# Optimization experiments

Hardware: AMD Instinct MI355X
Metric: run time of the kernel (lower is better)

Reference implementation:

```python
import jax, jax.numpy as jnp
import numpy as np

N = 50000   # num nodes
E = 800000  # num edges (avg degree 16)
D = 128     # in = hidden = out channels


def setup_inputs() -> dict:
    key = jax.random.key(0)
    k0, k1, k2, k3, k4, k5 = jax.random.split(key, 6)
    x = jax.random.normal(k0, (N, D), dtype=jnp.float32)
    edge_index = jax.random.randint(k1, (2, E), 0, N, dtype=jnp.int32)
    scale = 1.0 / np.sqrt(D)
    W1 = jax.random.normal(k2, (D, D), dtype=jnp.float32) * scale
    b1 = jax.random.normal(k3, (D,), dtype=jnp.float32) * 0.01
    W2 = jax.random.normal(k4, (D, D), dtype=jnp.float32) * scale
    b2 = jax.random.normal(k5, (D,), dtype=jnp.float32) * 0.01
    return {"x": x, "edge_index": edge_index, "W1": W1, "b1": b1, "W2": W2, "b2": b2}


def reference(x, edge_index, W1, b1, W2, b2):
    n = x.shape[0]
    src, dst = edge_index[0], edge_index[1]
    # GCN adds self-loops before normalization
    loops = jnp.arange(n, dtype=src.dtype)
    s = jnp.concatenate([src, loops])
    d = jnp.concatenate([dst, loops])
    # symmetric normalization: deg^{-1/2}[s] * deg^{-1/2}[d]
    deg = jax.ops.segment_sum(jnp.ones_like(d, dtype=x.dtype), d, num_segments=n)
    dinv = jnp.where(deg > 0, jax.lax.rsqrt(deg), 0.0)
    ew = dinv[s] * dinv[d]  # [E+N]

    def gcn_conv(h, W, b):
        h = h @ W                                   # [N, D] dense transform first
        msg = ew[:, None] * h[s]                     # gather over edges [E+N, D]
        agg = jax.ops.segment_sum(msg, d, num_segments=n)  # scatter-add [N, D]
        return agg + b

    # layer 1: conv -> Identity BN -> ELU (dropout=0.0 -> no-op)
    h = jax.nn.elu(gcn_conv(x, W1, b1))
    # layer 2 (last): conv -> Identity BN -> ELU
    out = jax.nn.elu(gcn_conv(h, W2, b2))
    return out
```

## Files before the change

### kernel.cpp

```cpp
#include <hip/hip_runtime.h>
#include <math.h>

#define D 128
#define BCAP 8192
#define SLICE 64
#define PB 256

typedef __attribute__((ext_vector_type(8))) short bf16x8;
typedef __attribute__((ext_vector_type(4))) float f32x4;


__device__ inline float2 bf2f2(unsigned int u) {
    union { unsigned int i; float f; } a, b;
    a.i = u << 16;
    b.i = u & 0xffff0000u;
    return make_float2(a.f, b.f);
}

__device__ inline unsigned short f2bf(float f) {
    union { float f; unsigned int i; } u;
    u.f = f;
    unsigned int r = u.i + 0x7fffu + ((u.i >> 16) & 1u);
    return (unsigned short)(r >> 16);
}


__device__ __forceinline__ void gemm_core(unsigned short (*Ws)[136], int gbid,
                                          const void* __restrict__ Ain, int a_fp32,
                                          unsigned int* __restrict__ Cb, int N) {
    const int tid = threadIdx.x;
    const int wid = tid >> 6;
    const int lane = tid & 63;
    const int quad = lane >> 4;
    const int ln = lane & 15;
    const int m = gbid * 64 + wid * 16 + ln;
    const bool valid = (m < N);

    f32x4 acc[8];
#pragma unroll
    for (int c = 0; c < 8; ++c) acc[c] = (f32x4){0.f, 0.f, 0.f, 0.f};

    __syncthreads();

#pragma unroll
    for (int ks = 0; ks < 4; ++ks) {
        const int k0 = ks * 32;
        bf16x8 af;
        if (a_fp32) {
            const float* A = (const float*)Ain;
            float4 lo = make_float4(0.f, 0.f, 0.f, 0.f), hi = lo;
            if (valid) {
                lo = *(const float4*)&A[(size_t)m * 128 + k0 + quad * 8];
                hi = *(const float4*)&A[(size_t)m * 128 + k0 + quad * 8 + 4];
            }
            af[0] = (short)f2bf(lo.x); af[1] = (short)f2bf(lo.y);
            af[2] = (short)f2bf(lo.z); af[3] = (short)f2bf(lo.w);
            af[4] = (short)f2bf(hi.x); af[5] = (short)f2bf(hi.y);
            af[6] = (short)f2bf(hi.z); af[7] = (short)f2bf(hi.w);
        } else {
            const uint4* A4 = (const uint4*)Ain;
            uint4 v = valid ? A4[(size_t)m * 16 + ks * 4 + quad]
                            : make_uint4(0u, 0u, 0u, 0u);
            union { uint4 u; bf16x8 h; } cv;
            cv.u = v;
            af = cv.h;
        }
#pragma unroll
        for (int c = 0; c < 8; ++c) {
            bf16x8 bf = *(const bf16x8*)&Ws[c * 16 + ln][k0 + quad * 8];
            acc[c] = __builtin_amdgcn_mfma_f32_16x16x32_bf16(af, bf, acc[c], 0, 0, 0);
        }
    }

    const int rowbase = gbid * 64 + wid * 16 + quad * 4;
#pragma unroll
    for (int c = 0; c < 8; ++c) {
#pragma unroll
        for (int r = 0; r < 4; ++r) {
            float v = acc[c][r];
            float vn = __shfl_xor(v, 1);
            int grow = rowbase + r;
            if (!(ln & 1) && grow < N) {
                unsigned int u = (unsigned int)f2bf(v) | ((unsigned int)f2bf(vn) << 16);
                Cb[(size_t)grow * 64 + c * 8 + (ln >> 1)] = u;
            }
        }
    }
}


__global__ __launch_bounds__(256) void k1_all(
        const int* __restrict__ src, const int* __restrict__ dst,
        const float* __restrict__ x, const float* __restrict__ W1,
        const float* __restrict__ W2, unsigned short* __restrict__ Wt2,
        unsigned int* __restrict__ pairs, unsigned char* __restrict__ cellCnt,
        unsigned int* __restrict__ hb1, int e, int chunk, int N, int gemmBlocks) {
    __shared__ __align__(16) unsigned char smem[128 * 136 * 2];
    const int tid = threadIdx.x;
    const int bid = blockIdx.x;

    if (bid < PB) {
        int* cur = (int*)smem;
        cur[tid] = 0;
        __syncthreads();
        const int e0 = bid * chunk;
        const int e1 = min(e0 + chunk, e);
        for (int i = e0 + tid; i < e1; i += 256) {
            int d = dst[i], s = src[i];
            int b = d >> 8;
            int off = atomicAdd(&cur[b], 1);
            if (off < SLICE)
                pairs[((size_t)(bid * 256 + b)) * SLICE + off] =
                    (unsigned int)s | ((unsigned int)(d & 255) << 16);
        }
        __syncthreads();
        cellCnt[bid * 256 + tid] = (unsigned char)min(cur[tid], SLICE);
    } else if (bid < PB + gemmBlocks) {
        unsigned short (*Ws)[136] = (unsigned short(*)[136])smem;
        for (int j = 0; j < 64; ++j) {
            int idx = tid + j * 256;
            Ws[idx & 127][idx >> 7] = f2bf(W1[idx]);
        }
        gemm_core(Ws, bid - PB, x, 1, hb1, N);
    } else {
        int i = (bid - PB - gemmBlocks) * 256 + tid;
        int k = i >> 7, n = i & 127;
        Wt2[n * 128 + k] = f2bf(W2[i]);
    }
}


__global__ __launch_bounds__(256) void partB(const unsigned int* __restrict__ pairs,
                                             const unsigned char* __restrict__ cellCnt,
                                             unsigned short* __restrict__ col,
                                             unsigned int* __restrict__ meta,
                                             float* __restrict__ dinv, int n) {
    __shared__ int deg[256];
    __shared__ int sc[256];
    __shared__ int cur[256];
    const int b = blockIdx.x;
    const int tid = threadIdx.x;

    deg[tid] = 0;
    __syncthreads();

    const int c = cellCnt[tid * 256 + b];
    const unsigned int* cell = pairs + ((size_t)(tid * 256 + b)) * SLICE;
    for (int q = 0; q < c; ++q) atomicAdd(&deg[cell[q] >> 16], 1);
    __syncthreads();

    int v = deg[tid];
    sc[tid] = v;
    __syncthreads();
    for (int o = 1; o < 256; o <<= 1) {
        int t = (tid >= o) ? sc[tid - o] : 0;
        __syncthreads();
        sc[tid] += t;
        __syncthreads();
    }
    int startw = sc[tid] - v;
    cur[tid] = startw;

    int node = b * 256 + tid;
    if (node < n) {
        meta[node] = ((unsigned int)(b * BCAP + startw) << 10) | (unsigned int)v;
        dinv[node] = rsqrtf((float)(v + 1));
    }
    __syncthreads();

    for (int q = 0; q < c; ++q) {
        unsigned int p = cell[q];
        int dl = p >> 16;
        int off = atomicAdd(&cur[dl], 1);
        col[(size_t)b * BCAP + off] = (unsigned short)(p & 0xffffu);
    }
}


__device__ __forceinline__ float2 agg_node(const unsigned int* __restrict__ hb,
                                           const unsigned int* __restrict__ meta,
                                           const unsigned short* __restrict__ col,
                                           const float* __restrict__ dinv,
                                           int node, int lane, float2 bv) {
    const float di = dinv[node];
    float2 self = bf2f2(hb[(size_t)node * 64 + lane]);
    float2 a0 = make_float2(di * self.x, di * self.y);
    float2 a1 = make_float2(0.f, 0.f), a2 = make_float2(0.f, 0.f),
           a3 = make_float2(0.f, 0.f), a4 = make_float2(0.f, 0.f),
           a5 = make_float2(0.f, 0.f), a6 = make_float2(0.f, 0.f),
           a7 = make_float2(0.f, 0.f);

    const unsigned int m = meta[node];
    const int s0 = (int)(m >> 10);
    const int s1 = s0 + (int)(m & 1023u);
    int i = s0;
    for (; i + 8 <= s1; i += 8) {
        int c0 = col[i + 0], c1 = col[i + 1], c2 = col[i + 2], c3 = col[i + 3];
        int c4 = col[i + 4], c5 = col[i + 5], c6 = col[i + 6], c7 = col[i + 7];
        float w0 = dinv[c0], w1 = dinv[c1], w2 = dinv[c2], w3 = dinv[c3];
        float w4 = dinv[c4], w5 = dinv[c5], w6 = dinv[c6], w7 = dinv[c7];
        unsigned int u0 = hb[(size_t)c0 * 64 + lane];
        unsigned int u1 = hb[(size_t)c1 * 64 + lane];
        unsigned int u2 = hb[(size_t)c2 * 64 + lane];
        unsigned int u3 = hb[(size_t)c3 * 64 + lane];
        unsigned int u4 = hb[(size_t)c4 * 64 + lane];
        unsigned int u5 = hb[(size_t)c5 * 64 + lane];
        unsigned int u6 = hb[(size_t)c6 * 64 + lane];
        unsigned int u7 = hb[(size_t)c7 * 64 + lane];
        float2 v0 = bf2f2(u0), v1 = bf2f2(u1), v2 = bf2f2(u2), v3 = bf2f2(u3);
        float2 v4 = bf2f2(u4), v5 = bf2f2(u5), v6 = bf2f2(u6), v7 = bf2f2(u7);
        a0.x = fmaf(w0, v0.x, a0.x); a0.y = fmaf(w0, v0.y, a0.y);
        a1.x = fmaf(w1, v1.x, a1.x); a1.y = fmaf(w1, v1.y, a1.y);
        a2.x = fmaf(w2, v2.x, a2.x); a2.y = fmaf(w2, v2.y, a2.y);
        a3.x = fmaf(w3, v3.x, a3.x); a3.y = fmaf(w3, v3.y, a3.y);
        a4.x = fmaf(w4, v4.x, a4.x); a4.y = fmaf(w4, v4.y, a4.y);
        a5.x = fmaf(w5, v5.x, a5.x); a5.y = fmaf(w5, v5.y, a5.y);
        a6.x = fmaf(w6, v6.x, a6.x); a6.y = fmaf(w6, v6.y, a6.y);
        a7.x = fmaf(w7, v7.x, a7.x); a7.y = fmaf(w7, v7.y, a7.y);
    }
    for (; i < s1; ++i) {
        int c = col[i];
        float ww = dinv[c];
        float2 v = bf2f2(hb[(size_t)c * 64 + lane]);
        a0.x = fmaf(ww, v.x, a0.x); a0.y = fmaf(ww, v.y, a0.y);
    }

    float sx = (a0.x + a1.x) + (a2.x + a3.x) + (a4.x + a5.x) + (a6.x + a7.x);
    float sy = (a0.y + a1.y) + (a2.y + a3.y) + (a4.y + a5.y) + (a6.y + a7.y);
    float rx = fmaf(di, sx, bv.x);
    float ry = fmaf(di, sy, bv.y);
    rx = rx > 0.0f ? rx : expm1f(rx);
    ry = ry > 0.0f ? ry : expm1f(ry);
    return make_float2(rx, ry);
}


__global__ __launch_bounds__(256) void k3_agg_gemm(
        const unsigned int* __restrict__ hb1, const unsigned int* __restrict__ meta,
        const unsigned short* __restrict__ col, const float* __restrict__ dinv,
        const float* __restrict__ b1, const unsigned short* __restrict__ Wt2,
        unsigned int* __restrict__ hb2, int n) {
    __shared__ unsigned int g1s[16 * 68];
    __shared__ __align__(16) unsigned short Ws[64][136];

    const int tid = threadIdx.x;
    const int wid = tid >> 6;
    const int lane = tid & 63;
    const int nodeBase = blockIdx.x * 16;
    const float2 bv = ((const float2*)b1)[lane];

    for (int t = 0; t < 4; ++t) {
        const int node = nodeBase + wid * 4 + t;
        unsigned int packed = 0;
        if (node < n) {
            float2 r = agg_node(hb1, meta, col, dinv, node, lane, bv);
            packed = (unsigned int)f2bf(r.x) | ((unsigned int)f2bf(r.y) << 16);
        }
        g1s[(wid * 4 + t) * 68 + lane] = packed;
    }
    __syncthreads();

    const int quad = lane >> 4;
    const int ln = lane & 15;

#pragma unroll
    for (int pass = 0; pass < 2; ++pass) {
        {
            int nloc = tid >> 2;
            int kb = (tid & 3) * 32;
            const uint4* g = (const uint4*)(Wt2 + (size_t)(pass * 64 + nloc) * 128 + kb);
            uint4* s = (uint4*)&Ws[nloc][kb];
            s[0] = g[0]; s[1] = g[1]; s[2] = g[2]; s[3] = g[3];
        }
        __syncthreads();

        f32x4 acc = (f32x4){0.f, 0.f, 0.f, 0.f};
#pragma unroll
        for (int ks = 0; ks < 4; ++ks) {
            bf16x8 af = *(const bf16x8*)&g1s[ln * 68 + ks * 16 + quad * 4];
            bf16x8 bf = *(const bf16x8*)&Ws[wid * 16 + ln][ks * 32 + quad * 8];
            acc = __builtin_amdgcn_mfma_f32_16x16x32_bf16(af, bf, acc, 0, 0, 0);
        }
        const int c = pass * 4 + wid;
#pragma unroll
        for (int r = 0; r < 4; ++r) {
            float v = acc[r];
            float vn = __shfl_xor(v, 1);
            int grow = nodeBase + quad * 4 + r;
            if (!(ln & 1) && grow < n) {
                hb2[(size_t)grow * 64 + c * 8 + (ln >> 1)] =
                    (unsigned int)f2bf(v) | ((unsigned int)f2bf(vn) << 16);
            }
        }
        __syncthreads();
    }
}


__global__ __launch_bounds__(256) void agg_elu(const unsigned int* __restrict__ hb,
                                               const unsigned int* __restrict__ meta,
                                               const unsigned short* __restrict__ col,
                                               const float* __restrict__ dinv,
                                               const float* __restrict__ bias,
                                               float* __restrict__ outf, int n) {
    const int wid = threadIdx.x >> 6;
    const int lane = threadIdx.x & 63;
    const int node = blockIdx.x * 4 + wid;
    if (node >= n) return;
    const float2 bv = ((const float2*)bias)[lane];
    float2 r = agg_node(hb, meta, col, dinv, node, lane, bv);
    ((float2*)outf)[(size_t)node * 64 + lane] = r;
}


extern "C" void kernel_launch(void* const* d_in, const int* in_sizes, int n_in,
                              void* d_out, int out_size, void* d_ws, size_t ws_size,
                              hipStream_t stream) {
    const float* x  = (const float*)d_in[0];
    const int*   ei = (const int*)d_in[1];
    const float* W1 = (const float*)d_in[2];
    const float* b1 = (const float*)d_in[3];
    const float* W2 = (const float*)d_in[4];
    const float* b2 = (const float*)d_in[5];
    float* out = (float*)d_out;

    const int N = in_sizes[0] / D;
    const int E = in_sizes[1] / 2;
    const int* src = ei;
    const int* dst = ei + E;
    const int NB = (N + 255) / 256;

    char* ws = (char*)d_ws;
    size_t off = 0;
    auto alloc = [&](size_t bytes) -> void* {
        void* p = ws + off;
        off = (off + bytes + 255) & ~(size_t)255;
        return p;
    };
    unsigned int*   pairs   = (unsigned int*)alloc((size_t)PB * 256 * SLICE * 4);
    unsigned char*  cellCnt = (unsigned char*)alloc((size_t)PB * 256);
    unsigned short* col     = (unsigned short*)alloc((size_t)NB * BCAP * 2);
    unsigned int*   meta    = (unsigned int*)alloc((size_t)N * 4);
    float*          dinv    = (float*)alloc((size_t)N * 4);
    unsigned short* Wt2     = (unsigned short*)alloc(128 * 128 * 2);
    unsigned int*   hb1     = (unsigned int*)alloc((size_t)N * 64 * 4);
    unsigned int*   hb2     = (unsigned int*)alloc((size_t)N * 64 * 4);
    (void)ws_size; (void)n_in; (void)out_size;

    const int chunk = (E + PB - 1) / PB;
    const int gemmBlocks = (N + 63) / 64;

    k1_all<<<PB + gemmBlocks + 64, 256, 0, stream>>>(src, dst, x, W1, W2, Wt2,
                                                     pairs, cellCnt, hb1, E, chunk,
                                                     N, gemmBlocks);
    partB<<<NB, 256, 0, stream>>>(pairs, cellCnt, col, meta, dinv, N);
    k3_agg_gemm<<<(N + 15) / 16, 256, 0, stream>>>(hb1, meta, col, dinv, b1, Wt2, hb2, N);
    agg_elu<<<(N + 3) / 4, 256, 0, stream>>>(hb2, meta, col, dinv, b2, out, N);
}
```

Measured before the change: 198.6 us.

## Fuse all GCN stages into one cooperative persistent kernel with grid syncs

Replaces the four separate launches with a single cooperative persistent kernel that walks each stage with grid-stride loops and separates stages with grid.sync(). The layer-2 GEMM is split out of the fused agg+GEMM kernel into its own phase, which writes the aggregated layer-1 result to a new g1 buffer. Weights are now converted to bf16 inside each GEMM tile in two 64-column passes, which removes the separate W2 transpose blocks. This saves launch gaps and tail effects, but adds grid-sync costs, an extra round trip of the intermediate through global memory, and repeated per-tile weight conversion. A multi-kernel fallback runs if the cooperative launch fails.

```diff
diff --git a/kernel.cpp b/kernel.cpp
--- a/kernel.cpp
+++ b/kernel.cpp
@@ -1,5 +1,8 @@
 #include <hip/hip_runtime.h>
+#include <hip/hip_cooperative_groups.h>
 #include <math.h>
+
+namespace cg = cooperative_groups;
 
 #define D 128
 #define BCAP 8192
@@ -25,9 +28,83 @@
 }
 
 
-__device__ __forceinline__ void gemm_core(unsigned short (*Ws)[136], int gbid,
-                                          const void* __restrict__ Ain, int a_fp32,
-                                          unsigned int* __restrict__ Cb, int N) {
+struct __align__(16) SMem {
+    union {
+        int cur[256];
+        struct { int deg[256]; int sc[256]; int cur2[256]; } pb;
+        unsigned short Ws[64][136];
+    };
+};
+
+
+__device__ __forceinline__ void partition_item(SMem& sm, int j,
+        const int* __restrict__ src, const int* __restrict__ dst,
+        unsigned int* __restrict__ pairs, unsigned char* __restrict__ cellCnt,
+        int e, int chunk) {
+    const int tid = threadIdx.x;
+    sm.cur[tid] = 0;
+    __syncthreads();
+    const int e0 = j * chunk;
+    const int e1 = min(e0 + chunk, e);
+    for (int i = e0 + tid; i < e1; i += 256) {
+        int d = dst[i], s = src[i];
+        int b = d >> 8;
+        int off = atomicAdd(&sm.cur[b], 1);
+        if (off < SLICE)
+            pairs[((size_t)(j * 256 + b)) * SLICE + off] =
+                (unsigned int)s | ((unsigned int)(d & 255) << 16);
+    }
+    __syncthreads();
+    cellCnt[j * 256 + tid] = (unsigned char)min(sm.cur[tid], SLICE);
+    __syncthreads();
+}
+
+
+__device__ __forceinline__ void partB_item(SMem& sm, int b,
+        const unsigned int* __restrict__ pairs, const unsigned char* __restrict__ cellCnt,
+        unsigned short* __restrict__ col, unsigned int* __restrict__ meta,
+        float* __restrict__ dinv, int n) {
+    const int tid = threadIdx.x;
+    sm.pb.deg[tid] = 0;
+    __syncthreads();
+
+    const int c = cellCnt[tid * 256 + b];
+    const unsigned int* cell = pairs + ((size_t)(tid * 256 + b)) * SLICE;
+    for (int q = 0; q < c; ++q) atomicAdd(&sm.pb.deg[cell[q] >> 16], 1);
+    __syncthreads();
+
+    int v = sm.pb.deg[tid];
+    sm.pb.sc[tid] = v;
+    __syncthreads();
+    for (int o = 1; o < 256; o <<= 1) {
+        int t = (tid >= o) ? sm.pb.sc[tid - o] : 0;
+        __syncthreads();
+        sm.pb.sc[tid] += t;
+        __syncthreads();
+    }
+    int startw = sm.pb.sc[tid] - v;
+    sm.pb.cur2[tid] = startw;
+
+    int node = b * 256 + tid;
+    if (node < n) {
+        meta[node] = ((unsigned int)(b * BCAP + startw) << 10) | (unsigned int)v;
+        dinv[node] = rsqrtf((float)(v + 1));
+    }
+    __syncthreads();
+
+    for (int q = 0; q < c; ++q) {
+        unsigned int p = cell[q];
+        int dl = p >> 16;
+        int off = atomicAdd(&sm.pb.cur2[dl], 1);
+        col[(size_t)b * BCAP + off] = (unsigned short)(p & 0xffffu);
+    }
+    __syncthreads();
+}
+
+
+__device__ __forceinline__ void gemm_tile(unsigned short (*Ws)[136], int gbid,
+        const void* __restrict__ Ain, int a_fp32, const float* __restrict__ W,
+        unsigned int* __restrict__ Cb, int N) {
     const int tid = threadIdx.x;
     const int wid = tid >> 6;
     const int lane = tid & 63;
@@ -36,143 +113,65 @@
     const int m = gbid * 64 + wid * 16 + ln;
     const bool valid = (m < N);
 
-    f32x4 acc[8];
-#pragma unroll
-    for (int c = 0; c < 8; ++c) acc[c] = (f32x4){0.f, 0.f, 0.f, 0.f};
-
-    __syncthreads();
-
-#pragma unroll
-    for (int ks = 0; ks < 4; ++ks) {
-        const int k0 = ks * 32;
-        bf16x8 af;
-        if (a_fp32) {
-            const float* A = (const float*)Ain;
-            float4 lo = make_float4(0.f, 0.f, 0.f, 0.f), hi = lo;
-            if (valid) {
-                lo = *(const float4*)&A[(size_t)m * 128 + k0 + quad * 8];
-                hi = *(const float4*)&A[(size_t)m * 128 + k0 + quad * 8 + 4];
+#pragma unroll
+    for (int pass = 0; pass < 2; ++pass) {
+        __syncthreads();
+#pragma unroll
+        for (int j = 0; j < 32; ++j) {
+            int idx = tid + j * 256;
+            int nl = idx & 63, k = idx >> 6;
+            Ws[nl][k] = f2bf(W[k * 128 + pass * 64 + nl]);
+        }
+        __syncthreads();
+
+        f32x4 acc[4];
+#pragma unroll
+        for (int c = 0; c < 4; ++c) acc[c] = (f32x4){0.f, 0.f, 0.f, 0.f};
+
+#pragma unroll
+        for (int ks = 0; ks < 4; ++ks) {
+            const int k0 = ks * 32;
+            bf16x8 af;
+            if (a_fp32) {
+                const float* A = (const float*)Ain;
+                float4 lo = make_float4(0.f, 0.f, 0.f, 0.f), hi = lo;
+                if (valid) {
+                    lo = *(const float4*)&A[(size_t)m * 128 + k0 + quad * 8];
+                    hi = *(const float4*)&A[(size_t)m * 128 + k0 + quad * 8 + 4];
+                }
+                af[0] = (short)f2bf(lo.x); af[1] = (short)f2bf(lo.y);
+                af[2] = (short)f2bf(lo.z); af[3] = (short)f2bf(lo.w);
+                af[4] = (short)f2bf(hi.x); af[5] = (short)f2bf(hi.y);
+                af[6] = (short)f2bf(hi.z); af[7] = (short)f2bf(hi.w);
+            } else {
+                const uint4* A4 = (const uint4*)Ain;
+                uint4 v = valid ? A4[(size_t)m * 16 + ks * 4 + quad]
+                                : make_uint4(0u, 0u, 0u, 0u);
+                union { uint4 u; bf16x8 h; } cv;
+                cv.u = v;
+                af = cv.h;
             }
-            af[0] = (short)f2bf(lo.x); af[1] = (short)f2bf(lo.y);
-            af[2] = (short)f2bf(lo.z); af[3] = (short)f2bf(lo.w);
-            af[4] = (short)f2bf(hi.x); af[5] = (short)f2bf(hi.y);
-            af[6] = (short)f2bf(hi.z); af[7] = (short)f2bf(hi.w);
-        } else {
-            const uint4* A4 = (const uint4*)Ain;
-            uint4 v = valid ? A4[(size_t)m * 16 + ks * 4 + quad]
-                            : make_uint4(0u, 0u, 0u, 0u);
-            union { uint4 u; bf16x8 h; } cv;
-            cv.u = v;
-            af = cv.h;
-        }
-#pragma unroll
-        for (int c = 0; c < 8; ++c) {
-            bf16x8 bf = *(const bf16x8*)&Ws[c * 16 + ln][k0 + quad * 8];
-            acc[c] = __builtin_amdgcn_mfma_f32_16x16x32_bf16(af, bf, acc[c], 0, 0, 0);
-        }
-    }
-
-    const int rowbase = gbid * 64 + wid * 16 + quad * 4;
-#pragma unroll
-    for (int c = 0; c < 8; ++c) {
-#pragma unroll
-        for (int r = 0; r < 4; ++r) {
-            float v = acc[c][r];
-            float vn = __shfl_xor(v, 1);
-            int grow = rowbase + r;
-            if (!(ln & 1) && grow < N) {
-                unsigned int u = (unsigned int)f2bf(v) | ((unsigned int)f2bf(vn) << 16);
-                Cb[(size_t)grow * 64 + c * 8 + (ln >> 1)] = u;
+#pragma unroll
+            for (int c = 0; c < 4; ++c) {
+                bf16x8 bf = *(const bf16x8*)&Ws[c * 16 + ln][k0 + quad * 8];
+                acc[c] = __builtin_amdgcn_mfma_f32_16x16x32_bf16(af, bf, acc[c], 0, 0, 0);
             }
         }
-    }
-}
-
-
-__global__ __launch_bounds__(256) void k1_all(
-        const int* __restrict__ src, const int* __restrict__ dst,
-        const float* __restrict__ x, const float* __restrict__ W1,
-        const float* __restrict__ W2, unsigned short* __restrict__ Wt2,
-        unsigned int* __restrict__ pairs, unsigned char* __restrict__ cellCnt,
-        unsigned int* __restrict__ hb1, int e, int chunk, int N, int gemmBlocks) {
-    __shared__ __align__(16) unsigned char smem[128 * 136 * 2];
-    const int tid = threadIdx.x;
-    const int bid = blockIdx.x;
-
-    if (bid < PB) {
-        int* cur = (int*)smem;
-        cur[tid] = 0;
-        __syncthreads();
-        const int e0 = bid * chunk;
-        const int e1 = min(e0 + chunk, e);
-        for (int i = e0 + tid; i < e1; i += 256) {
-            int d = dst[i], s = src[i];
-            int b = d >> 8;
-            int off = atomicAdd(&cur[b], 1);
-            if (off < SLICE)
-                pairs[((size_t)(bid * 256 + b)) * SLICE + off] =
-                    (unsigned int)s | ((unsigned int)(d & 255) << 16);
+
+        const int rowbase = gbid * 64 + wid * 16 + quad * 4;
+#pragma unroll
+        for (int c = 0; c < 4; ++c) {
+#pragma unroll
+            for (int r = 0; r < 4; ++r) {
+                float v = acc[c][r];
+                float vn = __shfl_xor(v, 1);
+                int grow = rowbase + r;
+                if (!(ln & 1) && grow < N) {
+                    Cb[(size_t)grow * 64 + (pass * 4 + c) * 8 + (ln >> 1)] =
+                        (unsigned int)f2bf(v) | ((unsigned int)f2bf(vn) << 16);
+                }
+            }
         }
-        __syncthreads();
-        cellCnt[bid * 256 + tid] = (unsigned char)min(cur[tid], SLICE);
-    } else if (bid < PB + gemmBlocks) {
-        unsigned short (*Ws)[136] = (unsigned short(*)[136])smem;
-        for (int j = 0; j < 64; ++j) {
-            int idx = tid + j * 256;
-            Ws[idx & 127][idx >> 7] = f2bf(W1[idx]);
-        }
-        gemm_core(Ws, bid - PB, x, 1, hb1, N);
-    } else {
-        int i = (bid - PB - gemmBlocks) * 256 + tid;
-        int k = i >> 7, n = i & 127;
-        Wt2[n * 128 + k] = f2bf(W2[i]);
-    }
-}
-
-
-__global__ __launch_bounds__(256) void partB(const unsigned int* __restrict__ pairs,
-                                             const unsigned char* __restrict__ cellCnt,
-                                             unsigned short* __restrict__ col,
-                                             unsigned int* __restrict__ meta,
-                                             float* __restrict__ dinv, int n) {
-    __shared__ int deg[256];
-    __shared__ int sc[256];
-    __shared__ int cur[256];
-    const int b = blockIdx.x;
-    const int tid = threadIdx.x;
-
-    deg[tid] = 0;
-    __syncthreads();
-
-    const int c = cellCnt[tid * 256 + b];
-    const unsigned int* cell = pairs + ((size_t)(tid * 256 + b)) * SLICE;
-    for (int q = 0; q < c; ++q) atomicAdd(&deg[cell[q] >> 16], 1);
-    __syncthreads();
-
-    int v = deg[tid];
-    sc[tid] = v;
-    __syncthreads();
-    for (int o = 1; o < 256; o <<= 1) {
-        int t = (tid >= o) ? sc[tid - o] : 0;
-        __syncthreads();
-        sc[tid] += t;
-        __syncthreads();
-    }
-    int startw = sc[tid] - v;
-    cur[tid] = startw;
-
-    int node = b * 256 + tid;
-    if (node < n) {
-        meta[node] = ((unsigned int)(b * BCAP + startw) << 10) | (unsigned int)v;
-        dinv[node] = rsqrtf((float)(v + 1));
-    }
-    __syncthreads();
-
-    for (int q = 0; q < c; ++q) {
-        unsigned int p = cell[q];
-        int dl = p >> 16;
-        int off = atomicAdd(&cur[dl], 1);
-        col[(size_t)b * BCAP + off] = (unsigned short)(p & 0xffffu);
     }
 }
 
@@ -235,74 +234,108 @@
 }
 
 
-__global__ __launch_bounds__(256) void k3_agg_gemm(
-        const unsigned int* __restrict__ hb1, const unsigned int* __restrict__ meta,
-        const unsigned short* __restrict__ col, const float* __restrict__ dinv,
-        const float* __restrict__ b1, const unsigned short* __restrict__ Wt2,
-        unsigned int* __restrict__ hb2, int n) {
-    __shared__ unsigned int g1s[16 * 68];
-    __shared__ __align__(16) unsigned short Ws[64][136];
-
-    const int tid = threadIdx.x;
-    const int wid = tid >> 6;
-    const int lane = tid & 63;
-    const int nodeBase = blockIdx.x * 16;
-    const float2 bv = ((const float2*)b1)[lane];
-
-    for (int t = 0; t < 4; ++t) {
-        const int node = nodeBase + wid * 4 + t;
-        unsigned int packed = 0;
-        if (node < n) {
-            float2 r = agg_node(hb1, meta, col, dinv, node, lane, bv);
-            packed = (unsigned int)f2bf(r.x) | ((unsigned int)f2bf(r.y) << 16);
-        }
-        g1s[(wid * 4 + t) * 68 + lane] = packed;
-    }
-    __syncthreads();
-
-    const int quad = lane >> 4;
-    const int ln = lane & 15;
-
-#pragma unroll
-    for (int pass = 0; pass < 2; ++pass) {
-        {
-            int nloc = tid >> 2;
-            int kb = (tid & 3) * 32;
-            const uint4* g = (const uint4*)(Wt2 + (size_t)(pass * 64 + nloc) * 128 + kb);
-            uint4* s = (uint4*)&Ws[nloc][kb];
-            s[0] = g[0]; s[1] = g[1]; s[2] = g[2]; s[3] = g[3];
-        }
-        __syncthreads();
-
-        f32x4 acc = (f32x4){0.f, 0.f, 0.f, 0.f};
-#pragma unroll
-        for (int ks = 0; ks < 4; ++ks) {
-            bf16x8 af = *(const bf16x8*)&g1s[ln * 68 + ks * 16 + quad * 4];
-            bf16x8 bf = *(const bf16x8*)&Ws[wid * 16 + ln][ks * 32 + quad * 8];
-            acc = __builtin_amdgcn_mfma_f32_16x16x32_bf16(af, bf, acc, 0, 0, 0);
-        }
-        const int c = pass * 4 + wid;
-#pragma unroll
-        for (int r = 0; r < 4; ++r) {
-            float v = acc[r];
-            float vn = __shfl_xor(v, 1);
-            int grow = nodeBase + quad * 4 + r;
-            if (!(ln & 1) && grow < n) {
-                hb2[(size_t)grow * 64 + c * 8 + (ln >> 1)] =
-                    (unsigned int)f2bf(v) | ((unsigned int)f2bf(vn) << 16);
+__global__ __launch_bounds__(256, 4) void mega(
+        const int* __restrict__ src, const int* __restrict__ dst,
+        const float* __restrict__ x, const float* __restrict__ W1,
+        const float* __restrict__ b1, const float* __restrict__ W2,
+        const float* __restrict__ b2, float* __restrict__ out,
+        unsigned int* __restrict__ pairs, unsigned char* __restrict__ cellCnt,
+        unsigned short* __restrict__ col, unsigned int* __restrict__ meta,
+        float* __restrict__ dinv, unsigned int* __restrict__ hb1,
+        unsigned int* __restrict__ g1, unsigned int* __restrict__ hb2,
+        int N, int E, int chunk, int gemmBlocks, int aggGroups, int nbuckets) {
+    __shared__ SMem sm;
+    cg::grid_group grid = cg::this_grid();
+    const int gsz = gridDim.x;
+    const int wid = threadIdx.x >> 6;
+    const int lane = threadIdx.x & 63;
+
+    const int p0 = PB + gemmBlocks;
+    for (int it = blockIdx.x; it < p0; it += gsz) {
+        if (it < PB) partition_item(sm, it, src, dst, pairs, cellCnt, E, chunk);
+        else         gemm_tile(sm.Ws, it - PB, x, 1, W1, hb1, N);
+    }
+    grid.sync();
+
+    for (int b = blockIdx.x; b < nbuckets; b += gsz)
+        partB_item(sm, b, pairs, cellCnt, col, meta, dinv, N);
+    grid.sync();
+
+    {
+        const float2 bv = ((const float2*)b1)[lane];
+        for (int grp = blockIdx.x; grp < aggGroups; grp += gsz) {
+            int node = grp * 4 + wid;
+            if (node < N) {
+                float2 r = agg_node(hb1, meta, col, dinv, node, lane, bv);
+                g1[(size_t)node * 64 + lane] =
+                    (unsigned int)f2bf(r.x) | ((unsigned int)f2bf(r.y) << 16);
             }
         }
-        __syncthreads();
-    }
-}
-
-
-__global__ __launch_bounds__(256) void agg_elu(const unsigned int* __restrict__ hb,
-                                               const unsigned int* __restrict__ meta,
-                                               const unsigned short* __restrict__ col,
-                                               const float* __restrict__ dinv,
-                                               const float* __restrict__ bias,
-                                               float* __restrict__ outf, int n) {
+    }
+    grid.sync();
+
+    for (int t = blockIdx.x; t < gemmBlocks; t += gsz)
+        gemm_tile(sm.Ws, t, g1, 0, W2, hb2, N);
+    grid.sync();
+
+    {
+        const float2 bv = ((const float2*)b2)[lane];
+        for (int grp = blockIdx.x; grp < aggGroups; grp += gsz) {
+            int node = grp * 4 + wid;
+            if (node < N) {
+                float2 r = agg_node(hb2, meta, col, dinv, node, lane, bv);
+                ((float2*)out)[(size_t)node * 64 + lane] = r;
+            }
+        }
+    }
+}
+
+
+__global__ __launch_bounds__(256) void fb_p0(
+        const int* __restrict__ src, const int* __restrict__ dst,
+        const float* __restrict__ x, const float* __restrict__ W1,
+        unsigned int* __restrict__ pairs, unsigned char* __restrict__ cellCnt,
+        unsigned int* __restrict__ hb1, int E, int chunk, int N) {
+    __shared__ SMem sm;
+    if ((int)blockIdx.x < PB)
+        partition_item(sm, blockIdx.x, src, dst, pairs, cellCnt, E, chunk);
+    else
+        gemm_tile(sm.Ws, blockIdx.x - PB, x, 1, W1, hb1, N);
+}
+
+__global__ __launch_bounds__(256) void fb_p1(
+        const unsigned int* __restrict__ pairs, const unsigned char* __restrict__ cellCnt,
+        unsigned short* __restrict__ col, unsigned int* __restrict__ meta,
+        float* __restrict__ dinv, int n) {
+    __shared__ SMem sm;
+    partB_item(sm, blockIdx.x, pairs, cellCnt, col, meta, dinv, n);
+}
+
+__global__ __launch_bounds__(256) void fb_p2(
+        const unsigned int* __restrict__ hb, const unsigned int* __restrict__ meta,
+        const unsigned short* __restrict__ col, const float* __restrict__ dinv,
+        const float* __restrict__ bias, unsigned int* __restrict__ outb, int n) {
+    const int wid = threadIdx.x >> 6;
+    const int lane = threadIdx.x & 63;
+    const int node = blockIdx.x * 4 + wid;
+    if (node >= n) return;
+    const float2 bv = ((const float2*)bias)[lane];
+    float2 r = agg_node(hb, meta, col, dinv, node, lane, bv);
+    outb[(size_t)node * 64 + lane] =
+        (unsigned int)f2bf(r.x) | ((unsigned int)f2bf(r.y) << 16);
+}
+
+__global__ __launch_bounds__(256) void fb_p3(
+        const unsigned int* __restrict__ g1, const float* __restrict__ W2,
+        unsigned int* __restrict__ hb2, int N) {
+    __shared__ SMem sm;
+    gemm_tile(sm.Ws, blockIdx.x, g1, 0, W2, hb2, N);
+}
+
+__global__ __launch_bounds__(256) void fb_p4(
+        const unsigned int* __restrict__ hb, const unsigned int* __restrict__ meta,
+        const unsigned short* __restrict__ col, const float* __restrict__ dinv,
+        const float* __restrict__ bias, float* __restrict__ outf, int n) {
     const int wid = threadIdx.x >> 6;
     const int lane = threadIdx.x & 63;
     const int node = blockIdx.x * 4 + wid;
@@ -324,11 +357,11 @@
     const float* b2 = (const float*)d_in[5];
     float* out = (float*)d_out;
 
-    const int N = in_sizes[0] / D;
-    const int E = in_sizes[1] / 2;
+    int N = in_sizes[0] / D;
+    int E = in_sizes[1] / 2;
     const int* src = ei;
     const int* dst = ei + E;
-    const int NB = (N + 255) / 256;
+    int nbuckets = (N + 255) / 256;
 
     char* ws = (char*)d_ws;
     size_t off = 0;
@@ -339,21 +372,45 @@
     };
     unsigned int*   pairs   = (unsigned int*)alloc((size_t)PB * 256 * SLICE * 4);
     unsigned char*  cellCnt = (unsigned char*)alloc((size_t)PB * 256);
-    unsigned short* col     = (unsigned short*)alloc((size_t)NB * BCAP * 2);
+    unsigned short* col     = (unsigned short*)alloc((size_t)nbuckets * BCAP * 2);
     unsigned int*   meta    = (unsigned int*)alloc((size_t)N * 4);
     float*          dinv    = (float*)alloc((size_t)N * 4);
-    unsigned short* Wt2     = (unsigned short*)alloc(128 * 128 * 2);
     unsigned int*   hb1     = (unsigned int*)alloc((size_t)N * 64 * 4);
+    unsigned int*   g1      = (unsigned int*)alloc((size_t)N * 64 * 4);
     unsigned int*   hb2     = (unsigned int*)alloc((size_t)N * 64 * 4);
     (void)ws_size; (void)n_in; (void)out_size;
 
-    const int chunk = (E + PB - 1) / PB;
-    const int gemmBlocks = (N + 63) / 64;
-
-    k1_all<<<PB + gemmBlocks + 64, 256, 0, stream>>>(src, dst, x, W1, W2, Wt2,
-                                                     pairs, cellCnt, hb1, E, chunk,
-                                                     N, gemmBlocks);
-    partB<<<NB, 256, 0, stream>>>(pairs, cellCnt, col, meta, dinv, N);
-    k3_agg_gemm<<<(N + 15) / 16, 256, 0, stream>>>(hb1, meta, col, dinv, b1, Wt2, hb2, N);
-    agg_elu<<<(N + 3) / 4, 256, 0, stream>>>(hb2, meta, col, dinv, b2, out, N);
-}
+    int chunk = (E + PB - 1) / PB;
+    int gemmBlocks = (N + 63) / 64;
+    int aggGroups = (N + 3) / 4;
+
+    int dev = 0;
+    hipGetDevice(&dev);
+    int numCU = 256;
+    hipDeviceGetAttribute(&numCU, hipDeviceAttributeMultiprocessorCount, dev);
+    int maxb = 0;
+    if (hipOccupancyMaxActiveBlocksPerMultiprocessor(&maxb, (const void*)mega, 256, 0)
+            != hipSuccess || maxb < 1)
+        maxb = 1;
+    if (maxb > 6) maxb = 6;
+    int grid = numCU * maxb;
+
+    void* args[] = {
+        (void*)&src, (void*)&dst, (void*)&x, (void*)&W1, (void*)&b1,
+        (void*)&W2, (void*)&b2, (void*)&out,
+        (void*)&pairs, (void*)&cellCnt, (void*)&col, (void*)&meta, (void*)&dinv,
+        (void*)&hb1, (void*)&g1, (void*)&hb2,
+        (void*)&N, (void*)&E, (void*)&chunk, (void*)&gemmBlocks,
+        (void*)&aggGroups, (void*)&nbuckets,
+    };
+    hipError_t err = hipLaunchCooperativeKernel((const void*)mega, dim3(grid), dim3(256),
+                                                args, 0, stream);
+    if (err != hipSuccess) {
+        fb_p0<<<PB + gemmBlocks, 256, 0, stream>>>(src, dst, x, W1, pairs, cellCnt,
+                                                   hb1, E, chunk, N);
+        fb_p1<<<nbuckets, 256, 0, stream>>>(pairs, cellCnt, col, meta, dinv, N);
+        fb_p2<<<aggGroups, 256, 0, stream>>>(hb1, meta, col, dinv, b1, g1, N);
+        fb_p3<<<gemmBlocks, 256, 0, stream>>>(g1, W2, hb2, N);
+        fb_p4<<<aggGroups, 256, 0, stream>>>(hb2, meta, col, dinv, b2, out, N);
+    }
+}
```

New measurement: 586.3 us. 2.95x slower.

## Split fused agg+GEMM into quarter-row aggregation kernel plus separate layer-2 GEMM

Applied to the files above, without the earlier changes.

Replaces the wave-per-node aggregation with a kernel where 16 lanes handle a quarter of a node's feature row, so each wave covers 4 nodes and each block covers 16 nodes times 4 feature quarters. The layer-1 aggregation and the layer-2 GEMM are unfused: the aggregated bf16 result goes to a new g1 buffer, then a separate GEMM kernel converts W2 and runs the shared gemm_core. The W2 transpose blocks are removed from k1_all. The aim is better lane utilization and occupancy during the gather. The cost is an extra launch and an extra N x 128 bf16 round-trip through global memory, and lanes in a wave now diverge across nodes with different degrees.

```diff
diff --git a/kernel.cpp b/kernel.cpp
--- a/kernel.cpp
+++ b/kernel.cpp
@@ -92,9 +92,8 @@
 __global__ __launch_bounds__(256) void k1_all(
         const int* __restrict__ src, const int* __restrict__ dst,
         const float* __restrict__ x, const float* __restrict__ W1,
-        const float* __restrict__ W2, unsigned short* __restrict__ Wt2,
         unsigned int* __restrict__ pairs, unsigned char* __restrict__ cellCnt,
-        unsigned int* __restrict__ hb1, int e, int chunk, int N, int gemmBlocks) {
+        unsigned int* __restrict__ hb1, int e, int chunk, int N) {
     __shared__ __align__(16) unsigned char smem[128 * 136 * 2];
     const int tid = threadIdx.x;
     const int bid = blockIdx.x;
@@ -115,17 +114,14 @@
         }
         __syncthreads();
         cellCnt[bid * 256 + tid] = (unsigned char)min(cur[tid], SLICE);
-    } else if (bid < PB + gemmBlocks) {
+    } else {
         unsigned short (*Ws)[136] = (unsigned short(*)[136])smem;
+#pragma unroll
         for (int j = 0; j < 64; ++j) {
             int idx = tid + j * 256;
             Ws[idx & 127][idx >> 7] = f2bf(W1[idx]);
         }
         gemm_core(Ws, bid - PB, x, 1, hb1, N);
-    } else {
-        int i = (bid - PB - gemmBlocks) * 256 + tid;
-        int k = i >> 7, n = i & 127;
-        Wt2[n * 128 + k] = f2bf(W2[i]);
     }
 }
 
@@ -177,36 +173,63 @@
 }
 
 
-__device__ __forceinline__ float2 agg_node(const unsigned int* __restrict__ hb,
-                                           const unsigned int* __restrict__ meta,
-                                           const unsigned short* __restrict__ col,
-                                           const float* __restrict__ dinv,
-                                           int node, int lane, float2 bv) {
-    const float di = dinv[node];
-    float2 self = bf2f2(hb[(size_t)node * 64 + lane]);
+__global__ __launch_bounds__(256) void agg_q(const unsigned int* __restrict__ hb,
+                                             const unsigned int* __restrict__ meta,
+                                             const unsigned short* __restrict__ col,
+                                             const float* __restrict__ dinv,
+                                             const float* __restrict__ bias,
+                                             float* __restrict__ outf,
+                                             unsigned int* __restrict__ outb,
+                                             int write_bf, int n) {
+    const int tid = threadIdx.x;
+    const int q = blockIdx.x & 3;
+    const int nodeBase = (blockIdx.x >> 2) * 16;
+    const int sub = tid >> 4;
+    const int l16 = tid & 15;
+    const int node = nodeBase + sub;
+    const int qoff = q * 16;
+    const bool nv = (node < n);
+
+    const unsigned int m = nv ? meta[node] : 0u;
+    const int s0 = (int)(m >> 10);
+    const int deg = (int)(m & 1023u);
+    const float di = nv ? dinv[node] : 0.f;
+
+    float2 self = nv ? bf2f2(hb[(size_t)node * 64 + qoff + l16]) : make_float2(0.f, 0.f);
     float2 a0 = make_float2(di * self.x, di * self.y);
     float2 a1 = make_float2(0.f, 0.f), a2 = make_float2(0.f, 0.f),
            a3 = make_float2(0.f, 0.f), a4 = make_float2(0.f, 0.f),
            a5 = make_float2(0.f, 0.f), a6 = make_float2(0.f, 0.f),
            a7 = make_float2(0.f, 0.f);
 
-    const unsigned int m = meta[node];
-    const int s0 = (int)(m >> 10);
-    const int s1 = s0 + (int)(m & 1023u);
-    int i = s0;
-    for (; i + 8 <= s1; i += 8) {
-        int c0 = col[i + 0], c1 = col[i + 1], c2 = col[i + 2], c3 = col[i + 3];
-        int c4 = col[i + 4], c5 = col[i + 5], c6 = col[i + 6], c7 = col[i + 7];
-        float w0 = dinv[c0], w1 = dinv[c1], w2 = dinv[c2], w3 = dinv[c3];
-        float w4 = dinv[c4], w5 = dinv[c5], w6 = dinv[c6], w7 = dinv[c7];
-        unsigned int u0 = hb[(size_t)c0 * 64 + lane];
-        unsigned int u1 = hb[(size_t)c1 * 64 + lane];
-        unsigned int u2 = hb[(size_t)c2 * 64 + lane];
-        unsigned int u3 = hb[(size_t)c3 * 64 + lane];
-        unsigned int u4 = hb[(size_t)c4 * 64 + lane];
-        unsigned int u5 = hb[(size_t)c5 * 64 + lane];
-        unsigned int u6 = hb[(size_t)c6 * 64 + lane];
-        unsigned int u7 = hb[(size_t)c7 * 64 + lane];
+    int i = 0;
+    while (__any(i < deg)) {
+        bool p0 = (i + 0) < deg, p1 = (i + 1) < deg, p2 = (i + 2) < deg, p3 = (i + 3) < deg;
+        bool p4 = (i + 4) < deg, p5 = (i + 5) < deg, p6 = (i + 6) < deg, p7 = (i + 7) < deg;
+        int c0 = p0 ? (int)col[s0 + i + 0] : 0;
+        int c1 = p1 ? (int)col[s0 + i + 1] : 0;
+        int c2 = p2 ? (int)col[s0 + i + 2] : 0;
+        int c3 = p3 ? (int)col[s0 + i + 3] : 0;
+        int c4 = p4 ? (int)col[s0 + i + 4] : 0;
+        int c5 = p5 ? (int)col[s0 + i + 5] : 0;
+        int c6 = p6 ? (int)col[s0 + i + 6] : 0;
+        int c7 = p7 ? (int)col[s0 + i + 7] : 0;
+        float w0 = p0 ? dinv[c0] : 0.f;
+        float w1 = p1 ? dinv[c1] : 0.f;
+        float w2 = p2 ? dinv[c2] : 0.f;
+        float w3 = p3 ? dinv[c3] : 0.f;
+        float w4 = p4 ? dinv[c4] : 0.f;
+        float w5 = p5 ? dinv[c5] : 0.f;
+        float w6 = p6 ? dinv[c6] : 0.f;
+        float w7 = p7 ? dinv[c7] : 0.f;
+        unsigned int u0 = hb[(size_t)c0 * 64 + qoff + l16];
+        unsigned int u1 = hb[(size_t)c1 * 64 + qoff + l16];
+        unsigned int u2 = hb[(size_t)c2 * 64 + qoff + l16];
+        unsigned int u3 = hb[(size_t)c3 * 64 + qoff + l16];
+        unsigned int u4 = hb[(size_t)c4 * 64 + qoff + l16];
+        unsigned int u5 = hb[(size_t)c5 * 64 + qoff + l16];
+        unsigned int u6 = hb[(size_t)c6 * 64 + qoff + l16];
+        unsigned int u7 = hb[(size_t)c7 * 64 + qoff + l16];
         float2 v0 = bf2f2(u0), v1 = bf2f2(u1), v2 = bf2f2(u2), v3 = bf2f2(u3);
         float2 v4 = bf2f2(u4), v5 = bf2f2(u5), v6 = bf2f2(u6), v7 = bf2f2(u7);
         a0.x = fmaf(w0, v0.x, a0.x); a0.y = fmaf(w0, v0.y, a0.y);
@@ -217,99 +240,36 @@
         a5.x = fmaf(w5, v5.x, a5.x); a5.y = fmaf(w5, v5.y, a5.y);
         a6.x = fmaf(w6, v6.x, a6.x); a6.y = fmaf(w6, v6.y, a6.y);
         a7.x = fmaf(w7, v7.x, a7.x); a7.y = fmaf(w7, v7.y, a7.y);
-    }
-    for (; i < s1; ++i) {
-        int c = col[i];
-        float ww = dinv[c];
-        float2 v = bf2f2(hb[(size_t)c * 64 + lane]);
-        a0.x = fmaf(ww, v.x, a0.x); a0.y = fmaf(ww, v.y, a0.y);
-    }
-
+        i += 8;
+    }
+
+    if (!nv) return;
+    float2 bv = ((const float2*)bias)[qoff + l16];
     float sx = (a0.x + a1.x) + (a2.x + a3.x) + (a4.x + a5.x) + (a6.x + a7.x);
     float sy = (a0.y + a1.y) + (a2.y + a3.y) + (a4.y + a5.y) + (a6.y + a7.y);
     float rx = fmaf(di, sx, bv.x);
     float ry = fmaf(di, sy, bv.y);
     rx = rx > 0.0f ? rx : expm1f(rx);
     ry = ry > 0.0f ? ry : expm1f(ry);
-    return make_float2(rx, ry);
-}
-
-
-__global__ __launch_bounds__(256) void k3_agg_gemm(
-        const unsigned int* __restrict__ hb1, const unsigned int* __restrict__ meta,
-        const unsigned short* __restrict__ col, const float* __restrict__ dinv,
-        const float* __restrict__ b1, const unsigned short* __restrict__ Wt2,
-        unsigned int* __restrict__ hb2, int n) {
-    __shared__ unsigned int g1s[16 * 68];
-    __shared__ __align__(16) unsigned short Ws[64][136];
-
-    const int tid = threadIdx.x;
-    const int wid = tid >> 6;
-    const int lane = tid & 63;
-    const int nodeBase = blockIdx.x * 16;
-    const float2 bv = ((const float2*)b1)[lane];
-
-    for (int t = 0; t < 4; ++t) {
-        const int node = nodeBase + wid * 4 + t;
-        unsigned int packed = 0;
-        if (node < n) {
-            float2 r = agg_node(hb1, meta, col, dinv, node, lane, bv);
-            packed = (unsigned int)f2bf(r.x) | ((unsigned int)f2bf(r.y) << 16);
-        }
-        g1s[(wid * 4 + t) * 68 + lane] = packed;
-    }
-    __syncthreads();
-
-    const int quad = lane >> 4;
-    const int ln = lane & 15;
-
-#pragma unroll
-    for (int pass = 0; pass < 2; ++pass) {
-        {
-            int nloc = tid >> 2;
-            int kb = (tid & 3) * 32;
-            const uint4* g = (const uint4*)(Wt2 + (size_t)(pass * 64 + nloc) * 128 + kb);
-            uint4* s = (uint4*)&Ws[nloc][kb];
-            s[0] = g[0]; s[1] = g[1]; s[2] = g[2]; s[3] = g[3];
-        }
-        __syncthreads();
-
-        f32x4 acc = (f32x4){0.f, 0.f, 0.f, 0.f};
-#pragma unroll
-        for (int ks = 0; ks < 4; ++ks) {
-            bf16x8 af = *(const bf16x8*)&g1s[ln * 68 + ks * 16 + quad * 4];
-            bf16x8 bf = *(const bf16x8*)&Ws[wid * 16 + ln][ks * 32 + quad * 8];
-            acc = __builtin_amdgcn_mfma_f32_16x16x32_bf16(af, bf, acc, 0, 0, 0);
-        }
-        const int c = pass * 4 + wid;
-#pragma unroll
-        for (int r = 0; r < 4; ++r) {
-            float v = acc[r];
-            float vn = __shfl_xor(v, 1);
-            int grow = nodeBase + quad * 4 + r;
-            if (!(ln & 1) && grow < n) {
-                hb2[(size_t)grow * 64 + c * 8 + (ln >> 1)] =
-                    (unsigned int)f2bf(v) | ((unsigned int)f2bf(vn) << 16);
-            }
-        }
-        __syncthreads();
-    }
-}
-
-
-__global__ __launch_bounds__(256) void agg_elu(const unsigned int* __restrict__ hb,
-                                               const unsigned int* __restrict__ meta,
-                                               const unsigned short* __restrict__ col,
-                                               const float* __restrict__ dinv,
-                                               const float* __restrict__ bias,
-                                               float* __restrict__ outf, int n) {
-    const int wid = threadIdx.x >> 6;
-    const int lane = threadIdx.x & 63;
-    const int node = blockIdx.x * 4 + wid;
-    if (node >= n) return;
-    const float2 bv = ((const float2*)bias)[lane];
-    float2 r = agg_node(hb, meta, col, dinv, node, lane, bv);
-    ((float2*)outf)[(size_t)node * 64 + lane] = r;
+    if (write_bf) {
+        outb[(size_t)node * 64 + qoff + l16] =
+            (unsigned int)f2bf(rx) | ((unsigned int)f2bf(ry) << 16);
+    } else {
+        ((float2*)outf)[(size_t)node * 64 + qoff + l16] = make_float2(rx, ry);
+    }
+}
+
+
+__global__ __launch_bounds__(256) void gemm_l2(const unsigned int* __restrict__ g1,
+                                               const float* __restrict__ W2,
+                                               unsigned int* __restrict__ hb2, int N) {
+    __shared__ __align__(16) unsigned short Ws[128][136];
+#pragma unroll
+    for (int j = 0; j < 64; ++j) {
+        int idx = threadIdx.x + j * 256;
+        Ws[idx & 127][idx >> 7] = f2bf(W2[idx]);
+    }
+    gemm_core(Ws, blockIdx.x, g1, 0, hb2, N);
 }
 
 
@@ -342,18 +302,19 @@
     unsigned short* col     = (unsigned short*)alloc((size_t)NB * BCAP * 2);
     unsigned int*   meta    = (unsigned int*)alloc((size_t)N * 4);
     float*          dinv    = (float*)alloc((size_t)N * 4);
-    unsigned short* Wt2     = (unsigned short*)alloc(128 * 128 * 2);
     unsigned int*   hb1     = (unsigned int*)alloc((size_t)N * 64 * 4);
+    unsigned int*   g1      = (unsigned int*)alloc((size_t)N * 64 * 4);
     unsigned int*   hb2     = (unsigned int*)alloc((size_t)N * 64 * 4);
     (void)ws_size; (void)n_in; (void)out_size;
 
     const int chunk = (E + PB - 1) / PB;
     const int gemmBlocks = (N + 63) / 64;
-
-    k1_all<<<PB + gemmBlocks + 64, 256, 0, stream>>>(src, dst, x, W1, W2, Wt2,
-                                                     pairs, cellCnt, hb1, E, chunk,
-                                                     N, gemmBlocks);
+    const int aggQBlocks = 4 * ((N + 15) / 16);
+
+    k1_all<<<PB + gemmBlocks, 256, 0, stream>>>(src, dst, x, W1, pairs, cellCnt,
+                                                hb1, E, chunk, N);
     partB<<<NB, 256, 0, stream>>>(pairs, cellCnt, col, meta, dinv, N);
-    k3_agg_gemm<<<(N + 15) / 16, 256, 0, stream>>>(hb1, meta, col, dinv, b1, Wt2, hb2, N);
-    agg_elu<<<(N + 3) / 4, 256, 0, stream>>>(hb2, meta, col, dinv, b2, out, N);
-}
+    agg_q<<<aggQBlocks, 256, 0, stream>>>(hb1, meta, col, dinv, b1, nullptr, g1, 1, N);
+    gemm_l2<<<gemmBlocks, 256, 0, stream>>>(g1, W2, hb2, N);
+    agg_q<<<aggQBlocks, 256, 0, stream>>>(hb2, meta, col, dinv, b2, out, nullptr, 0, N);
+}
```

Result: slower. 263.5 us (+32.7%).
